# Kernel tuning notes

Measured on AMD Instinct MI355X. Metric: run time of the kernel, lower is better.

## Reference

```python
import jax, jax.numpy as jnp
import numpy as np

D_MODEL = 1024
D_STATE = 16
D_CONV = 4
EXPAND = 2
D_INNER = EXPAND * D_MODEL          # 2048
DT_RANK = D_INNER // 16             # 128
BATCH = 2
SEQLEN = 1024


def _silu(x):
    return x * jax.nn.sigmoid(x)


def setup_inputs() -> dict:
    key = jax.random.key(0)
    ks = jax.random.split(key, 8)
    s = 0.02
    A_init = jnp.tile(jnp.arange(1, D_STATE + 1, dtype=jnp.float32)[None, :], (D_INNER, 1))
    return {
        "x": jax.random.normal(ks[0], (BATCH, SEQLEN, D_MODEL), jnp.float32),
        "W_in": jax.random.normal(ks[1], (D_MODEL, 2 * D_INNER), jnp.float32) * s,
        "conv_k": jax.random.normal(ks[2], (D_CONV, 1, D_INNER), jnp.float32) * s,  # (kw, in/groups, out)
        "conv_b": jnp.zeros((D_INNER,), jnp.float32),
        "W_xproj": jax.random.normal(ks[3], (D_INNER, DT_RANK + 2 * D_STATE), jnp.float32) * s,
        "W_dt": jax.random.normal(ks[4], (DT_RANK, D_INNER), jnp.float32) * s,
        "b_dt": jnp.zeros((D_INNER,), jnp.float32),
        "A_log": jnp.log(A_init),
        "D": jnp.ones((D_INNER,), jnp.float32),
        "W_out": jax.random.normal(ks[5], (D_INNER, D_MODEL), jnp.float32) * s,
    }


def reference(x, W_in, conv_k, conv_b, W_xproj, W_dt, b_dt, A_log, D, W_out):
    # in_proj and gate split
    xz = x @ W_in                                   # (B, L, 2*Di)
    x_in, z = jnp.split(xz, 2, axis=-1)             # each (B, L, Di)

    # depthwise causal conv1d: left-pad by d_conv-1 (keras padding='causal')
    xp = jnp.pad(x_in, ((0, 0), (D_CONV - 1, 0), (0, 0)))
    x_in = jax.lax.conv_general_dilated(
        xp, conv_k, window_strides=(1,), padding='VALID',
        dimension_numbers=('NWC', 'WIO', 'NWC'),
        feature_group_count=D_INNER) + conv_b
    u = _silu(x_in)                                 # (B, L, Di)

    # input-dependent SSM params
    x_dbl = u @ W_xproj                             # (B, L, dt_rank + 2*N)
    dt_low, Bm, Cm = jnp.split(x_dbl, [DT_RANK, DT_RANK + D_STATE], axis=-1)
    dt = jax.nn.softplus(dt_low @ W_dt + b_dt)      # (B, L, Di)
    A = -jnp.exp(A_log)                             # (Di, N)
    dA = jnp.exp(jnp.einsum('bld,dn->bldn', dt, A)) # (B, L, Di, N)
    dB = jnp.einsum('bld,bln->bldn', dt, Bm)        # (B, L, Di, N)

    # selective scan over sequence length
    def step(h, e):
        a_t, b_t, u_t, c_t = e                      # (B,Di,N), (B,Di,N), (B,Di), (B,N)
        h = a_t * h + b_t * u_t[..., None]
        y_t = jnp.einsum('bdn,bn->bd', h, c_t)
        return h, y_t

    h0 = jnp.zeros((x.shape[0], D_INNER, D_STATE), dtype=x.dtype)
    xs = (jnp.swapaxes(dA, 0, 1), jnp.swapaxes(dB, 0, 1),
          jnp.swapaxes(u, 0, 1), jnp.swapaxes(Cm, 0, 1))
    _, yT = jax.lax.scan(step, h0, xs)              # (L, B, Di)
    y = jnp.swapaxes(yT, 0, 1) + u * D              # skip connection

    return (y * _silu(z)) @ W_out                   # (B, L, d_model)
```

## Files before the change

kernel.cpp:

```cpp
#include <hip/hip_runtime.h>
#include <hip/hip_bf16.h>

#define D_MODEL 1024
#define D_STATE 16
#define D_CONV 4
#define D_INNER 2048
#define DT_RANK 128
#define BATCH 2
#define SEQLEN 1024
#define XCOLS 160
#define NCHUNK 32
#define LCHUNK 32

typedef __hip_bfloat16 bf16;
typedef __attribute__((ext_vector_type(8))) short short8;
typedef __attribute__((ext_vector_type(4))) float f32x4;

__device__ __forceinline__ unsigned short f2bf_bits(float f) {
    bf16 h = __float2bfloat16(f);
    return *(unsigned short*)&h;
}

__device__ __forceinline__ float bfbits2f(short s) {
    union { float f; unsigned u; } v;
    v.u = ((unsigned)(unsigned short)s) << 16;
    return v.f;
}

__device__ __forceinline__ float softplus_f(float x) {
    return fmaxf(x, 0.f) + __logf(1.f + __expf(-fabsf(x)));
}

__device__ __forceinline__ float silu_f(float x) {
    return x / (1.f + __expf(-x));
}

__device__ __forceinline__ void load16_lds(void* lds, const void* g) {
    __builtin_amdgcn_global_load_lds(
        (const __attribute__((address_space(1))) unsigned int*)g,
        (__attribute__((address_space(3))) unsigned int*)lds, 16, 0, 0);
}

__device__ __forceinline__ void transpose_tile(const float* __restrict__ B,
                                               bf16* __restrict__ Bt,
                                               int K, int N, int nt, int kt,
                                               float (*t)[33], int tid)
{
    const int tx = tid & 31, ty = tid >> 5;
    const int n0 = nt * 32, k0 = kt * 32;
    #pragma unroll
    for (int r = 0; r < 4; ++r) {
        int n = n0 + tx;
        t[ty + r * 8][tx] = (n < N) ? B[(size_t)(k0 + ty + r * 8) * N + n] : 0.f;
    }
    __syncthreads();
    #pragma unroll
    for (int r = 0; r < 4; ++r)
        Bt[(size_t)(n0 + ty + r * 8) * K + k0 + tx] = __float2bfloat16(t[tx][ty + r * 8]);
}

__global__ __launch_bounds__(256)
void prep_kernel(const float* __restrict__ x, bf16* __restrict__ x_bf,
                 const float* __restrict__ W_in, bf16* __restrict__ Win_t,
                 const float* __restrict__ W_xproj, bf16* __restrict__ Wxp_t,
                 const float* __restrict__ W_dt, bf16* __restrict__ Wdt_t,
                 const float* __restrict__ W_out, bf16* __restrict__ Wout_t,
                 const float* __restrict__ A_log, float* __restrict__ Aneg)
{
    __shared__ float t[32][33];
    const int tid = threadIdx.x;
    int blk = blockIdx.x;
    if (blk < 4096) {
        transpose_tile(W_in, Win_t, D_MODEL, 2 * D_INNER, blk & 127, blk >> 7, t, tid);
        return;
    }
    blk -= 4096;
    if (blk < 512) {
        transpose_tile(W_xproj, Wxp_t, D_INNER, XCOLS, blk & 7, blk >> 3, t, tid);
        return;
    }
    blk -= 512;
    if (blk < 256) {
        transpose_tile(W_dt, Wdt_t, DT_RANK, D_INNER, blk & 63, blk >> 6, t, tid);
        return;
    }
    blk -= 256;
    if (blk < 2048) {
        transpose_tile(W_out, Wout_t, D_INNER, D_MODEL, blk & 31, blk >> 5, t, tid);
        return;
    }
    blk -= 2048;
    if (blk < 2048) {
        int i = blk * 256 + tid;
        float4 v = ((const float4*)x)[i];
        ushort4 p;
        p.x = f2bf_bits(v.x); p.y = f2bf_bits(v.y);
        p.z = f2bf_bits(v.z); p.w = f2bf_bits(v.w);
        ((ushort4*)x_bf)[i] = p;
        return;
    }
    blk -= 2048;
    {
        int i = blk * 256 + tid;
        Aneg[i] = -__expf(A_log[i]);
    }
}

template<int BN, int EPI>
__global__ __launch_bounds__(256)
void gemm_mfma(const bf16* __restrict__ A, const bf16* __restrict__ Bt,
               float* __restrict__ C, bf16* __restrict__ Cb,
               bf16* __restrict__ Cb2,
               const float* __restrict__ bias,
               int M, int N, int K, int ldc, int kchunk)
{
    constexpr int WN = (BN == 128) ? 64 : 32;
    constexpr int NJ = WN / 16;
    __shared__ short As[128 * 32];
    __shared__ short Bs[BN * 32];
    const int tid = threadIdx.x;
    const int lane = tid & 63, wave = tid >> 6;
    const int wm = (wave >> 1) * 64, wn = (wave & 1) * WN;
    const int row0 = blockIdx.y * 128, col0 = blockIdx.x * BN;
    const int r_m = lane & 15, r_q = lane >> 4;
    const int kstart = blockIdx.z * kchunk;
    float* Cz = C + (size_t)blockIdx.z * M * ldc;

    const int srow = tid >> 2, schk = (tid & 3) * 8;
    const bf16* Ag0 = A  + (size_t)(row0 + srow)      * K + kstart + schk;
    const bf16* Ag1 = A  + (size_t)(row0 + srow + 64) * K + kstart + schk;
    const bf16* Bg0 = Bt + (size_t)(col0 + srow)      * K + kstart + schk;
    const bf16* Bg1 = Bt + (size_t)(col0 + srow + 64) * K + kstart + schk;
    short* AsW0 = &As[8 * tid];
    short* AsW1 = &As[8 * tid + 2048];
    short* BsW0 = &Bs[8 * tid];
    short* BsW1 = &Bs[8 * tid + 2048];

    f32x4 acc[4][NJ];
    #pragma unroll
    for (int i = 0; i < 4; ++i)
        #pragma unroll
        for (int j = 0; j < NJ; ++j)
            #pragma unroll
            for (int r = 0; r < 4; ++r) acc[i][j][r] = 0.f;

    for (int k0 = 0; k0 < kchunk; k0 += 32) {
        __syncthreads();
        load16_lds(AsW0, Ag0 + k0);
        load16_lds(AsW1, Ag1 + k0);
        load16_lds(BsW0, Bg0 + k0);
        if (BN == 128) load16_lds(BsW1, Bg1 + k0);
        __syncthreads();
        short8 af[4], bfr[NJ];
        #pragma unroll
        for (int i = 0; i < 4; ++i)
            af[i] = *(const short8*)&As[(wm + i * 16 + r_m) * 32 + r_q * 8];
        #pragma unroll
        for (int j = 0; j < NJ; ++j)
            bfr[j] = *(const short8*)&Bs[(wn + j * 16 + r_m) * 32 + r_q * 8];
        #pragma unroll
        for (int i = 0; i < 4; ++i)
            #pragma unroll
            for (int j = 0; j < NJ; ++j)
                acc[i][j] = __builtin_amdgcn_mfma_f32_16x16x32_bf16(
                    af[i], bfr[j], acc[i][j], 0, 0, 0);
    }

    #pragma unroll
    for (int i = 0; i < 4; ++i) {
        #pragma unroll
        for (int j = 0; j < NJ; ++j) {
            int row = row0 + wm + i * 16 + r_q * 4;
            int col = col0 + wn + j * 16 + r_m;
            if (col < N) {
                if (EPI == 1) {
                    float bv = bias[col];
                    #pragma unroll
                    for (int r = 0; r < 4; ++r)
                        Cb[(size_t)(row + r) * ldc + col] =
                            __float2bfloat16(softplus_f(acc[i][j][r] + bv));
                } else if (EPI == 2) {
                    if (col < 2048) {
                        #pragma unroll
                        for (int r = 0; r < 4; ++r)
                            Cb2[(size_t)(row + r) * ldc + col] =
                                __float2bfloat16(acc[i][j][r]);
                    } else {
                        int zc = col - 2048;
                        #pragma unroll
                        for (int r = 0; r < 4; ++r)
                            Cb[(size_t)(row + r) * ldc + zc] =
                                __float2bfloat16(silu_f(acc[i][j][r]));
                    }
                } else {
                    #pragma unroll
                    for (int r = 0; r < 4; ++r)
                        Cz[(size_t)(row + r) * ldc + col] = acc[i][j][r];
                }
            }
        }
    }
}

__global__ __launch_bounds__(256)
void reduce_xdbl(const float* __restrict__ Cpart, float* __restrict__ x_dbl,
                 bf16* __restrict__ dtA_bf)
{
    int i4 = blockIdx.x * 256 + threadIdx.x;
    if (i4 >= 2048 * (XCOLS / 4)) return;
    int r = i4 / (XCOLS / 4), c4 = i4 - r * (XCOLS / 4);
    float4 s = {0.f, 0.f, 0.f, 0.f};
    #pragma unroll
    for (int z = 0; z < 8; ++z) {
        float4 v = *(const float4*)&Cpart[(size_t)z * 2048 * 256 + (size_t)r * 256 + c4 * 4];
        s.x += v.x; s.y += v.y; s.z += v.z; s.w += v.w;
    }
    *(float4*)&x_dbl[(size_t)r * XCOLS + c4 * 4] = s;
    if (c4 < DT_RANK / 4) {
        ushort4 p;
        p.x = f2bf_bits(s.x); p.y = f2bf_bits(s.y);
        p.z = f2bf_bits(s.z); p.w = f2bf_bits(s.w);
        *(ushort4*)&dtA_bf[(size_t)r * DT_RANK + c4 * 4] = p;
    }
}

__global__ __launch_bounds__(256)
void reduce_out(const float* __restrict__ Cpart, float* __restrict__ out)
{
    int i = blockIdx.x * 256 + threadIdx.x;
    const float4* p0 = (const float4*)Cpart;
    const float4* p1 = p0 + (size_t)2048 * 1024 / 4;
    float4 a = p0[i], b = p1[i];
    float4 r; r.x = a.x + b.x; r.y = a.y + b.y; r.z = a.z + b.z; r.w = a.w + b.w;
    ((float4*)out)[i] = r;
}

__global__ __launch_bounds__(256)
void conv_silu_kernel(const bf16* __restrict__ xd,
                      const float* __restrict__ conv_k,
                      const float* __restrict__ conv_b,
                      bf16* __restrict__ u_bf)
{
    int idx8 = blockIdx.x * 256 + threadIdx.x;
    int d8 = idx8 & (D_INNER / 8 - 1);
    int t = (idx8 >> 8) & (SEQLEN - 1);
    int b = idx8 >> 18;
    float acc[8];
    {
        float4 b0 = ((const float4*)conv_b)[d8 * 2];
        float4 b1 = ((const float4*)conv_b)[d8 * 2 + 1];
        acc[0] = b0.x; acc[1] = b0.y; acc[2] = b0.z; acc[3] = b0.w;
        acc[4] = b1.x; acc[5] = b1.y; acc[6] = b1.z; acc[7] = b1.w;
    }
    #pragma unroll
    for (int k = 0; k < D_CONV; ++k) {
        int tt = t + k - (D_CONV - 1);
        if (tt >= 0) {
            short8 xv = ((const short8*)xd)[(size_t)(b * SEQLEN + tt) * (D_INNER / 8) + d8];
            float4 k0 = ((const float4*)conv_k)[k * (D_INNER / 4) + d8 * 2];
            float4 k1 = ((const float4*)conv_k)[k * (D_INNER / 4) + d8 * 2 + 1];
            acc[0] = fmaf(bfbits2f(xv[0]), k0.x, acc[0]);
            acc[1] = fmaf(bfbits2f(xv[1]), k0.y, acc[1]);
            acc[2] = fmaf(bfbits2f(xv[2]), k0.z, acc[2]);
            acc[3] = fmaf(bfbits2f(xv[3]), k0.w, acc[3]);
            acc[4] = fmaf(bfbits2f(xv[4]), k1.x, acc[4]);
            acc[5] = fmaf(bfbits2f(xv[5]), k1.y, acc[5]);
            acc[6] = fmaf(bfbits2f(xv[6]), k1.z, acc[6]);
            acc[7] = fmaf(bfbits2f(xv[7]), k1.w, acc[7]);
        }
    }
    short8 r;
    #pragma unroll
    for (int j = 0; j < 8; ++j)
        r[j] = (short)f2bf_bits(acc[j] / (1.f + __expf(-acc[j])));
    ((short8*)u_bf)[idx8] = r;
}

__global__ __launch_bounds__(256)
void scan_phase1(const bf16* __restrict__ dt_sb,
                 const float* __restrict__ Aneg,
                 const bf16* __restrict__ u_bf,
                 const float* __restrict__ x_dbl,
                 float* __restrict__ Pst, float* __restrict__ Sst)
{
    __shared__ float Bsm[LCHUNK][16];
    const int d = blockIdx.x * 256 + threadIdx.x;
    const int c = blockIdx.y, b = blockIdx.z;
    const int t0 = c * LCHUNK;
    for (int i = threadIdx.x; i < LCHUNK * 16; i += 256) {
        int tt = i >> 4, n = i & 15;
        Bsm[tt][n] = x_dbl[(size_t)(b * SEQLEN + t0 + tt) * XCOLS + DT_RANK + n];
    }
    float A_row[D_STATE];
    const float4* a4 = (const float4*)(Aneg + d * D_STATE);
    #pragma unroll
    for (int q = 0; q < 4; ++q) {
        float4 v = a4[q];
        A_row[q*4+0] = v.x; A_row[q*4+1] = v.y; A_row[q*4+2] = v.z; A_row[q*4+3] = v.w;
    }
    __syncthreads();
    float P[D_STATE], S[D_STATE];
    #pragma unroll
    for (int n = 0; n < D_STATE; ++n) { P[n] = 1.f; S[n] = 0.f; }
    const bf16* dpp = dt_sb + (size_t)(b * SEQLEN + t0) * D_INNER + d;
    const bf16* upp = u_bf + (size_t)(b * SEQLEN + t0) * D_INNER + d;
    #pragma unroll 4
    for (int t = 0; t < LCHUNK; ++t) {
        float dtv = __bfloat162float(dpp[(size_t)t * D_INNER]);
        float du = dtv * __bfloat162float(upp[(size_t)t * D_INNER]);
        const float4* b4 = (const float4*)&Bsm[t][0];
        #pragma unroll
        for (int q = 0; q < 4; ++q) {
            float4 v = b4[q];
            float Bn[4] = {v.x, v.y, v.z, v.w};
            #pragma unroll
            for (int e = 0; e < 4; ++e) {
                int n = q * 4 + e;
                float a = __expf(dtv * A_row[n]);
                P[n] *= a;
                S[n] = fmaf(a, S[n], du * Bn[e]);
            }
        }
    }
    const size_t base = ((size_t)(b * NCHUNK + c) * D_STATE) * D_INNER + d;
    #pragma unroll
    for (int n = 0; n < D_STATE; ++n) {
        Pst[base + (size_t)n * D_INNER] = P[n];
        Sst[base + (size_t)n * D_INNER] = S[n];
    }
}

__global__ __launch_bounds__(256)
void scan_phase2(const float* __restrict__ Pst, float* __restrict__ Sst)
{
    const int d = blockIdx.x * 256 + threadIdx.x;
    const int n = blockIdx.y;
    const int b = blockIdx.z;
    float h = 0.f;
    for (int c = 0; c < NCHUNK; ++c) {
        const size_t idx = ((size_t)(b * NCHUNK + c) * D_STATE + n) * D_INNER + d;
        float Pv = Pst[idx], Sv = Sst[idx];
        Sst[idx] = h;
        h = fmaf(Pv, h, Sv);
    }
}

__global__ __launch_bounds__(256)
void scan_phase3(const bf16* __restrict__ dt_sb,
                 const float* __restrict__ Aneg,
                 const bf16* __restrict__ u_bf,
                 const float* __restrict__ x_dbl,
                 const float* __restrict__ Dvec,
                 const bf16* __restrict__ sz_bf,
                 const float* __restrict__ hin,
                 bf16* __restrict__ g_bf)
{
    __shared__ float BCs[LCHUNK][32];
    const int d = blockIdx.x * 256 + threadIdx.x;
    const int c = blockIdx.y, b = blockIdx.z;
    const int t0 = c * LCHUNK;
    for (int i = threadIdx.x; i < LCHUNK * 32; i += 256) {
        int tt = i >> 5, col = i & 31;
        BCs[tt][col] = x_dbl[(size_t)(b * SEQLEN + t0 + tt) * XCOLS + DT_RANK + col];
    }
    float A_row[D_STATE];
    const float4* a4 = (const float4*)(Aneg + d * D_STATE);
    #pragma unroll
    for (int q = 0; q < 4; ++q) {
        float4 v = a4[q];
        A_row[q*4+0] = v.x; A_row[q*4+1] = v.y; A_row[q*4+2] = v.z; A_row[q*4+3] = v.w;
    }
    const float Dd = Dvec[d];
    __syncthreads();
    float h[D_STATE];
    const size_t base = ((size_t)(b * NCHUNK + c) * D_STATE) * D_INNER + d;
    #pragma unroll
    for (int n = 0; n < D_STATE; ++n) h[n] = hin[base + (size_t)n * D_INNER];
    const bf16* dpp = dt_sb + (size_t)(b * SEQLEN + t0) * D_INNER + d;
    const bf16* upp = u_bf + (size_t)(b * SEQLEN + t0) * D_INNER + d;
    const bf16* zpp = sz_bf + (size_t)(b * SEQLEN + t0) * D_INNER + d;
    bf16* gpp = g_bf + (size_t)(b * SEQLEN + t0) * D_INNER + d;
    #pragma unroll 4
    for (int t = 0; t < LCHUNK; ++t) {
        float dtv = __bfloat162float(dpp[(size_t)t * D_INNER]);
        float uv = __bfloat162float(upp[(size_t)t * D_INNER]);
        float sz = __bfloat162float(zpp[(size_t)t * D_INNER]);
        float du = dtv * uv;
        float y = 0.f;
        const float4* bc4 = (const float4*)&BCs[t][0];
        #pragma unroll
        for (int q = 0; q < 4; ++q) {
            float4 v = bc4[q];
            float4 w = bc4[q + 4];
            float Bn[4] = {v.x, v.y, v.z, v.w};
            float Cn[4] = {w.x, w.y, w.z, w.w};
            #pragma unroll
            for (int e = 0; e < 4; ++e) {
                int n = q * 4 + e;
                float a = __expf(dtv * A_row[n]);
                h[n] = fmaf(a, h[n], du * Bn[e]);
                y = fmaf(h[n], Cn[e], y);
            }
        }
        float gy = y + uv * Dd;
        gpp[(size_t)t * D_INNER] = __float2bfloat16(gy * sz);
    }
}

extern "C" void kernel_launch(void* const* d_in, const int* in_sizes, int n_in,
                              void* d_out, int out_size, void* d_ws, size_t ws_size,
                              hipStream_t stream)
{
    const float* x      = (const float*)d_in[0];
    const float* W_in   = (const float*)d_in[1];
    const float* conv_k = (const float*)d_in[2];
    const float* conv_b = (const float*)d_in[3];
    const float* W_xproj= (const float*)d_in[4];
    const float* W_dt   = (const float*)d_in[5];
    const float* b_dt   = (const float*)d_in[6];
    const float* A_log  = (const float*)d_in[7];
    const float* Dvec   = (const float*)d_in[8];
    const float* W_out  = (const float*)d_in[9];
    float* out = (float*)d_out;

    const int BL = BATCH * SEQLEN;

    float* ws     = (float*)d_ws;
    float* x_dbl  = ws;
    float* Pst    = x_dbl + (size_t)BL * XCOLS;
    float* Sst    = Pst + (size_t)BATCH * NCHUNK * D_STATE * D_INNER;
    float* Aneg   = Sst + (size_t)BATCH * NCHUNK * D_STATE * D_INNER;
    float* Cpart  = Aneg + 32768;
    bf16*  x_bf   = (bf16*)Cpart;
    bf16* Win_t  = (bf16*)(Cpart + (size_t)4 * 1048576);
    bf16* xd_bf  = Win_t + (size_t)4096 * 1024;
    bf16* u_bf   = xd_bf + (size_t)BL * D_INNER;
    bf16* sz_bf  = u_bf  + (size_t)BL * D_INNER;
    bf16* Wxp_t  = sz_bf + (size_t)BL * D_INNER;
    bf16* dtA_bf = Wxp_t + (size_t)256 * 2048;
    bf16* Wdt_t  = dtA_bf+ (size_t)BL * DT_RANK;
    bf16* g_bf   = Wdt_t + (size_t)2048 * 128;
    bf16* Wout_t = g_bf  + (size_t)BL * D_INNER;
    bf16* dt_sb  = Wout_t+ (size_t)1024 * 2048;

    prep_kernel<<<4096 + 512 + 256 + 2048 + 2048 + 128, 256, 0, stream>>>(
        x, x_bf, W_in, Win_t, W_xproj, Wxp_t, W_dt, Wdt_t, W_out, Wout_t, A_log, Aneg);

    gemm_mfma<128, 2><<<dim3(32, 16, 1), 256, 0, stream>>>(
        x_bf, Win_t, nullptr, sz_bf, xd_bf, nullptr, BL, 2 * D_INNER, D_MODEL, D_INNER, D_MODEL);

    conv_silu_kernel<<<(BL * D_INNER / 8) / 256, 256, 0, stream>>>(xd_bf, conv_k, conv_b, u_bf);

    gemm_mfma<64, 0><<<dim3(3, 16, 8), 256, 0, stream>>>(
        u_bf, Wxp_t, Cpart, nullptr, nullptr, nullptr, BL, 256, D_INNER, 256, 256);
    reduce_xdbl<<<(BL * (XCOLS / 4) + 255) / 256, 256, 0, stream>>>(Cpart, x_dbl, dtA_bf);

    gemm_mfma<64, 1><<<dim3(32, 16, 1), 256, 0, stream>>>(
        dtA_bf, Wdt_t, nullptr, dt_sb, nullptr, b_dt, BL, D_INNER, DT_RANK, D_INNER, DT_RANK);

    scan_phase1<<<dim3(D_INNER / 256, NCHUNK, BATCH), 256, 0, stream>>>(
        dt_sb, Aneg, u_bf, x_dbl, Pst, Sst);
    scan_phase2<<<dim3(D_INNER / 256, D_STATE, BATCH), 256, 0, stream>>>(Pst, Sst);
    scan_phase3<<<dim3(D_INNER / 256, NCHUNK, BATCH), 256, 0, stream>>>(
        dt_sb, Aneg, u_bf, x_dbl, Dvec, sz_bf, Sst, g_bf);

    gemm_mfma<64, 0><<<dim3(16, 16, 2), 256, 0, stream>>>(
        g_bf, Wout_t, Cpart, nullptr, nullptr, nullptr, BL, D_MODEL, D_INNER, D_MODEL, D_INNER / 2);
    reduce_out<<<(BL * D_MODEL / 4) / 256, 256, 0, stream>>>(Cpart, out);
}
```

Before: 237.6 us.

## Double-buffer GEMM LDS tiles, XOR-swizzle LDS layout, and remap blocks across XCDs

The bf16 MFMA GEMM now keeps two LDS buffers, so the global-to-LDS load of the next K slice is issued before computing on the current slice, with one barrier per slice instead of two. LDS columns are XOR-swizzled by row to reduce bank conflicts on the fragment reads. Block indices are permuted so consecutive hardware block ids spread across the 8 XCDs and neighbouring tiles share L2. The changes double LDS use, which may lower occupancy, and the loop assumes kchunk is a multiple of 64.

```diff
diff --git a/kernel.cpp b/kernel.cpp
--- a/kernel.cpp
+++ b/kernel.cpp
@@ -116,25 +116,34 @@
 {
     constexpr int WN = (BN == 128) ? 64 : 32;
     constexpr int NJ = WN / 16;
-    __shared__ short As[128 * 32];
-    __shared__ short Bs[BN * 32];
+    __shared__ short As[2][128 * 32];
+    __shared__ short Bs[2][BN * 32];
     const int tid = threadIdx.x;
     const int lane = tid & 63, wave = tid >> 6;
     const int wm = (wave >> 1) * 64, wn = (wave & 1) * WN;
-    const int row0 = blockIdx.y * 128, col0 = blockIdx.x * BN;
+
+    const int gx = gridDim.x, gy = gridDim.y;
+    const int total = gx * gy * gridDim.z;
+    const int hwid = (blockIdx.z * gy + blockIdx.y) * gx + blockIdx.x;
+    const int nid = (hwid & 7) * (total >> 3) + (hwid >> 3);
+    const int bz = nid / (gx * gy);
+    const int rem = nid - bz * (gx * gy);
+    const int bx = rem / gy;
+    const int by = rem - bx * gy;
+
+    const int row0 = by * 128, col0 = bx * BN;
     const int r_m = lane & 15, r_q = lane >> 4;
-    const int kstart = blockIdx.z * kchunk;
-    float* Cz = C + (size_t)blockIdx.z * M * ldc;
-
-    const int srow = tid >> 2, schk = (tid & 3) * 8;
+    const int kstart = bz * kchunk;
+    float* Cz = C + (size_t)bz * M * ldc;
+
+    const int srow = tid >> 2;
+    const int schk = ((tid & 3) ^ (srow & 3)) * 8;
     const bf16* Ag0 = A  + (size_t)(row0 + srow)      * K + kstart + schk;
     const bf16* Ag1 = A  + (size_t)(row0 + srow + 64) * K + kstart + schk;
     const bf16* Bg0 = Bt + (size_t)(col0 + srow)      * K + kstart + schk;
     const bf16* Bg1 = Bt + (size_t)(col0 + srow + 64) * K + kstart + schk;
-    short* AsW0 = &As[8 * tid];
-    short* AsW1 = &As[8 * tid + 2048];
-    short* BsW0 = &Bs[8 * tid];
-    short* BsW1 = &Bs[8 * tid + 2048];
+
+    const int cx = (r_q ^ (r_m & 3)) * 8;
 
     f32x4 acc[4][NJ];
     #pragma unroll
@@ -144,27 +153,43 @@
             #pragma unroll
             for (int r = 0; r < 4; ++r) acc[i][j][r] = 0.f;
 
-    for (int k0 = 0; k0 < kchunk; k0 += 32) {
+#define GEMM_STAGE(BUF, KOFF)                                                   \
+    {                                                                           \
+        load16_lds(&As[BUF][8 * tid], Ag0 + (KOFF));                            \
+        load16_lds(&As[BUF][8 * tid + 2048], Ag1 + (KOFF));                     \
+        load16_lds(&Bs[BUF][8 * tid], Bg0 + (KOFF));                            \
+        if (BN == 128) load16_lds(&Bs[BUF][8 * tid + 2048], Bg1 + (KOFF));      \
+    }
+
+#define GEMM_COMPUTE(BUF)                                                       \
+    {                                                                           \
+        short8 af[4], bfr[NJ];                                                  \
+        _Pragma("unroll")                                                       \
+        for (int i = 0; i < 4; ++i)                                             \
+            af[i] = *(const short8*)&As[BUF][(wm + i * 16 + r_m) * 32 + cx];    \
+        _Pragma("unroll")                                                       \
+        for (int j = 0; j < NJ; ++j)                                            \
+            bfr[j] = *(const short8*)&Bs[BUF][(wn + j * 16 + r_m) * 32 + cx];   \
+        _Pragma("unroll")                                                       \
+        for (int i = 0; i < 4; ++i)                                             \
+            _Pragma("unroll")                                                   \
+            for (int j = 0; j < NJ; ++j)                                        \
+                acc[i][j] = __builtin_amdgcn_mfma_f32_16x16x32_bf16(            \
+                    af[i], bfr[j], acc[i][j], 0, 0, 0);                         \
+    }
+
+    GEMM_STAGE(0, 0);
+    __syncthreads();
+    for (int k0 = 0; k0 < kchunk; k0 += 64) {
+        GEMM_STAGE(1, k0 + 32);
+        GEMM_COMPUTE(0);
         __syncthreads();
-        load16_lds(AsW0, Ag0 + k0);
-        load16_lds(AsW1, Ag1 + k0);
-        load16_lds(BsW0, Bg0 + k0);
-        if (BN == 128) load16_lds(BsW1, Bg1 + k0);
+        if (k0 + 64 < kchunk) GEMM_STAGE(0, k0 + 64);
+        GEMM_COMPUTE(1);
         __syncthreads();
-        short8 af[4], bfr[NJ];
-        #pragma unroll
-        for (int i = 0; i < 4; ++i)
-            af[i] = *(const short8*)&As[(wm + i * 16 + r_m) * 32 + r_q * 8];
-        #pragma unroll
-        for (int j = 0; j < NJ; ++j)
-            bfr[j] = *(const short8*)&Bs[(wn + j * 16 + r_m) * 32 + r_q * 8];
-        #pragma unroll
-        for (int i = 0; i < 4; ++i)
-            #pragma unroll
-            for (int j = 0; j < NJ; ++j)
-                acc[i][j] = __builtin_amdgcn_mfma_f32_16x16x32_bf16(
-                    af[i], bfr[j], acc[i][j], 0, 0, 0);
-    }
+    }
+#undef GEMM_STAGE
+#undef GEMM_COMPUTE
 
     #pragma unroll
     for (int i = 0; i < 4; ++i) {
```

After: 228.5 us. 3.8% less time.
